# Kernel tuning notes

Measured on AMD Instinct MI355X. Metric: run time of the kernel, lower is better.

## Reference

```python
import jax, jax.numpy as jnp
import numpy as np

H = 8          # num_head
HD = 64        # head_dim = hidden_dim // num_head
WIN = 33       # atten_window_size (odd)
MIN_SCORE = -1e9


def setup_inputs() -> dict:
    key = jax.random.key(0)
    ks = jax.random.split(key, 12)
    B, S, D = 8, 4096, 512
    scale = 1.0 / np.sqrt(D).astype(np.float32)

    def lin_w(k):
        return jax.random.normal(k, (D, D), jnp.float32) * scale

    return {
        "query": jax.random.normal(ks[0], (B, S, D), jnp.float32),
        "key": jax.random.normal(ks[1], (B, S, D), jnp.float32),
        "value": jax.random.normal(ks[2], (B, S, D), jnp.float32),
        "mask": jax.random.randint(ks[3], (B, S), 0, 2).astype(bool),
        "Wq": lin_w(ks[4]), "bq": jax.random.normal(ks[5], (D,), jnp.float32) * 0.02,
        "Wk": lin_w(ks[6]), "bk": jax.random.normal(ks[7], (D,), jnp.float32) * 0.02,
        "Wv": lin_w(ks[8]), "bv": jax.random.normal(ks[9], (D,), jnp.float32) * 0.02,
        "Wo": lin_w(ks[10]), "bo": jax.random.normal(ks[11], (D,), jnp.float32) * 0.02,
    }


def reference(query, key, value, mask, Wq, bq, Wk, bk, Wv, bv, Wo, bo):
    B, S, D = query.shape
    half = min(WIN // 2, S // 2)

    def proj_split(x, W, b):
        # nn.Linear: x @ W.T + b; then split heads and flatten (B,H) -> B*H
        y = x @ W.T + b
        return y.reshape(B, S, H, HD).transpose(0, 2, 1, 3).reshape(B * H, S, HD)

    q = proj_split(query, Wq, bq)   # [BH, S, HD]
    k = proj_split(key, Wk, bk)
    v = proj_split(value, Wv, bv)
    # mask expanded over heads; True = masked (LocalAttention semantics)
    m = jnp.broadcast_to(mask[:, None, :], (B, H, S)).reshape(B * H, S)

    # banded scores: one [BH, S] vector per window offset (no sqrt(head_dim) scaling,
    # faithful to LocalAttention)
    scores = []
    for off in range(-half, half + 1):
        if off < 0:
            w = jnp.sum(q[:, -off:] * k[:, :off], axis=-1)
            w = jnp.where(m[:, :off], MIN_SCORE, w)
            w = jnp.pad(w, ((0, 0), (-off, 0)), constant_values=MIN_SCORE)
        elif off == 0:
            w = jnp.where(m, MIN_SCORE, jnp.sum(q * k, axis=-1))
        else:
            w = jnp.sum(q[:, :-off] * k[:, off:], axis=-1)
            w = jnp.where(m[:, off:], MIN_SCORE, w)
            w = jnp.pad(w, ((0, 0), (0, off)), constant_values=MIN_SCORE)
        scores.append(w)
    probs = jax.nn.softmax(jnp.stack(scores, axis=-1), axis=-1)  # [BH, S, 2*half+1]

    # weighted gather of values along the band (dropout=0 -> identity)
    out = jnp.zeros_like(v)
    for i, off in enumerate(range(-half, half + 1)):
        p = probs[:, :, i:i + 1]
        if off < 0:
            out = out + jnp.pad(p[:, -off:] * v[:, :off], ((0, 0), (-off, 0), (0, 0)))
        elif off == 0:
            out = out + p * v
        else:
            out = out + jnp.pad(p[:, :-off] * v[:, off:], ((0, 0), (0, off), (0, 0)))

    out = out.reshape(B, H, S, HD).transpose(0, 2, 1, 3).reshape(B, S, D)
    return out @ Wo.T + bo
```

## Files before the change

### kernel.cpp

```cpp
#include <hip/hip_runtime.h>
#include <hip/hip_bf16.h>
#include <stdint.h>

#define BB 8
#define SS 4096
#define DD 512
#define HH 8
#define HDIM 64

typedef unsigned short u16;
typedef __attribute__((ext_vector_type(4))) float f32x4;
typedef __attribute__((ext_vector_type(4))) short s16x4;
typedef __attribute__((ext_vector_type(8))) short s16x8;
typedef __attribute__((ext_vector_type(4))) unsigned int u32x4;

__device__ __forceinline__ u16 f2bf(float f) {
  uint32_t x = __builtin_bit_cast(uint32_t, f);
  x += 0x7fffu + ((x >> 16) & 1u);
  return (u16)(x >> 16);
}
__device__ __forceinline__ float bf2f(u16 u) {
  uint32_t x = (uint32_t)u << 16;
  return __builtin_bit_cast(float, x);
}
__device__ __forceinline__ uint32_t cvtpk(float a, float b) {
  uint32_t d;
  asm("v_cvt_pk_bf16_f32 %0, %1, %2" : "=v"(d) : "v"(a), "v"(b));
  return d;
}

__device__ __forceinline__ void gld_lds16(const void* g, void* l) {
  __builtin_amdgcn_global_load_lds((const __attribute__((address_space(1))) void*)g,
                                   (__attribute__((address_space(3))) void*)l, 16, 0, 0);
}

__global__ void cvt_weights(const float* __restrict__ w0, const float* __restrict__ w1,
                            const float* __restrict__ w2, const float* __restrict__ w3,
                            u16* __restrict__ out) {
  int i = blockIdx.x * blockDim.x + threadIdx.x;
  const int n = DD * DD;
  if (i < n) {
    out[i]         = f2bf(w0[i]);
    out[n + i]     = f2bf(w1[i]);
    out[2 * n + i] = f2bf(w2[i]);
    out[3 * n + i] = f2bf(w3[i]);
  }
}

__global__ void mask_unpack(const void* __restrict__ mraw, uint8_t* __restrict__ mk, int n) {
  __shared__ int bad[3];
  __shared__ int mode;
  const int t = threadIdx.x;
  if (t < 3) bad[t] = 0;
  __syncthreads();
  const uint32_t* w = (const uint32_t*)mraw;
  const uint32_t x = w[t];
  const bool w01 = (x == 0u) || (x == 1u);
  const uint32_t ob = x | (x >> 8) | (x >> 16) | (x >> 24);
  const bool u01 = ((ob & 0xFEu) == 0u);
  if (!w01) atomicAdd(&bad[0], 1);
  if (!u01) atomicAdd(&bad[1], 1);
  __syncthreads();
  if (t == 0) mode = (bad[0] == 0) ? 0 : (bad[1] == 0 ? 1 : 2);
  __syncthreads();
  const int md = mode;
  for (int i = blockIdx.x * 256 + t; i < n; i += gridDim.x * 256) {
    uint8_t v;
    if (md == 0)      v = (uint8_t)(w[i] & 1u);
    else if (md == 1) v = ((const uint8_t*)mraw)[i] ? 1 : 0;
    else              v = (w[i] != 0u) ? 1 : 0;
    mk[i] = v;
  }
}

template <typename TA, typename TC>
__global__ __launch_bounds__(256, 2)
void gemm97(const TA* __restrict__ A, const u16* __restrict__ Bw,
            const float* __restrict__ bias, TC* __restrict__ C,
            int M, int N, int K) {
  constexpr bool AF32 = (sizeof(TA) == 4);
  constexpr int ABYTES = AF32 ? 128 * 64 * 4 : 128 * 64 * 2;
  __shared__ __align__(16) char sA[ABYTES];
  __shared__ __align__(16) u16 sB[128 * 64];

  const int tid = threadIdx.x;
  const int lane = tid & 63, wv = tid >> 6;
  const int wr = (wv >> 1) * 64, wc = (wv & 1) * 64;
  const int c = lane & 15, g = lane >> 4;
  const int lid = blockIdx.x;
  const int rb = (lid >> 5) * 8 + (lid & 7);
  const int cb = (lid >> 3) & 3;
  const int col0 = cb * 128, row0 = rb * 128;

  const int srB = tid >> 3, cBc = (tid & 7) ^ ((tid >> 3) & 7);
  const u16* b_src = Bw + (size_t)(col0 + srB) * K + cBc * 8;
  const int srA = tid >> 4, cAc = (tid & 15) ^ (tid >> 4);
  const TA* a_srcF = A + (size_t)(row0 + srA) * K + cAc * 4;
  const TA* a_srcH = A + (size_t)(row0 + srB) * K + cBc * 8;

  f32x4 acc[4][4];
#pragma unroll
  for (int a = 0; a < 4; ++a)
#pragma unroll
    for (int b = 0; b < 4; ++b) acc[a][b] = (f32x4){0.f, 0.f, 0.f, 0.f};

  const int nkt = K / 64;
  for (int kt = 0; kt < nkt; ++kt) {
    __syncthreads();
    const int ko = kt * 64;
    if constexpr (AF32) {
#pragma unroll
      for (int i = 0; i < 8; ++i)
        gld_lds16(a_srcF + (size_t)i * 16 * K + ko, sA + i * 4096 + wv * 1024);
    } else {
#pragma unroll
      for (int i = 0; i < 4; ++i)
        gld_lds16(a_srcH + (size_t)i * 32 * K + ko, sA + i * 4096 + wv * 1024);
    }
#pragma unroll
    for (int i = 0; i < 4; ++i)
      gld_lds16(b_src + (size_t)i * 32 * K + ko, (char*)sB + i * 4096 + wv * 1024);
    __syncthreads();

#pragma unroll
    for (int ks = 0; ks < 2; ++ks) {
      s16x8 af[4], bq[4];
#pragma unroll
      for (int mf = 0; mf < 4; ++mf) {
        const int row = wr + mf * 16 + c;
        if constexpr (AF32) {
          const int bc = ks * 128 + g * 32;
          const f32x4 lo4 = *(const f32x4*)(sA + row * 256 + ((bc) ^ (c << 4)));
          const f32x4 hi4 = *(const f32x4*)(sA + row * 256 + ((bc + 16) ^ (c << 4)));
          const u32x4 dd = (u32x4){cvtpk(lo4[0], lo4[1]), cvtpk(lo4[2], lo4[3]),
                                   cvtpk(hi4[0], hi4[1]), cvtpk(hi4[2], hi4[3])};
          af[mf] = __builtin_bit_cast(s16x8, dd);
        } else {
          const int bc = ks * 64 + g * 16;
          af[mf] = *(const s16x8*)(sA + row * 128 + (bc ^ ((c & 7) << 4)));
        }
      }
#pragma unroll
      for (int nf = 0; nf < 4; ++nf) {
        const int row = wc + nf * 16 + c;
        const int bc = ks * 64 + g * 16;
        bq[nf] = *(const s16x8*)((char*)sB + row * 128 + (bc ^ ((c & 7) << 4)));
      }
#pragma unroll
      for (int mf = 0; mf < 4; ++mf)
#pragma unroll
        for (int nf = 0; nf < 4; ++nf)
          acc[mf][nf] = __builtin_amdgcn_mfma_f32_16x16x32_bf16(af[mf], bq[nf], acc[mf][nf], 0, 0, 0);
    }
  }

#pragma unroll
  for (int nf = 0; nf < 4; ++nf) {
    const int col = col0 + wc + nf * 16 + c;
    const float bv = bias[col];
#pragma unroll
    for (int mf = 0; mf < 4; ++mf) {
#pragma unroll
      for (int i = 0; i < 4; ++i) {
        const int row = row0 + wr + mf * 16 + g * 4 + i;
        const float v = acc[mf][nf][i] + bv;
        if constexpr (sizeof(TC) == 4) C[(size_t)row * N + col] = v;
        else                           C[(size_t)row * N + col] = (TC)f2bf(v);
      }
    }
  }
}

__device__ __forceinline__ void hilo8(const f32x4& a0, const f32x4& a1, s16x8& h, s16x8& l) {
#pragma unroll
  for (int j = 0; j < 4; ++j) {
    const float f = a0[j];
    const u16 hb = f2bf(f);
    h[j] = (short)hb;
    l[j] = (short)f2bf(f - bf2f(hb));
  }
#pragma unroll
  for (int j = 0; j < 4; ++j) {
    const float f = a1[j];
    const u16 hb = f2bf(f);
    h[4 + j] = (short)hb;
    l[4 + j] = (short)f2bf(f - bf2f(hb));
  }
}

#define ACH 4

__global__ __launch_bounds__(256, 4)
void attn_mfma(const float* __restrict__ Qp, const float* __restrict__ Kp,
               const u16* __restrict__ Vp, const uint8_t* __restrict__ mk,
               u16* __restrict__ O) {
  __shared__ u16 sKh[96 * 72];
  __shared__ u16 sKl[96 * 68];
  __shared__ u16 sVT[64 * 104];
  __shared__ u16 sM[96];

  const int bh = blockIdx.x;
  const int b = bh >> 3, h = bh & 7;
  const int base0 = blockIdx.y * (64 * ACH);
  const int tid = threadIdx.x;

  const int wv = tid >> 6, lane = tid & 63;
  const int c = lane & 15, g = lane >> 4;
  const int qloc = wv * 16 + c;

  const int krow0 = tid >> 3, kj = tid & 7;
  const int kks = kj >> 2, kg2 = kj & 3;
  const int vk0 = tid >> 3, vdg8 = tid & 7;

  f32x4 kA0[3], kA1[3];
  s16x8 vR[3];
  u16 mR = 1;
  f32x4 qn0[2], qn1[2];

  auto issue_loads = [&](int cs) {
#pragma unroll
    for (int it = 0; it < 3; ++it) {
      const int row = krow0 + it * 32;
      const int gr = cs - 16 + row;
      if (gr >= 0 && gr < SS) {
        const float* kp = Kp + ((size_t)(b * SS + gr)) * DD + h * HDIM + kks * 32 + kg2 * 4;
        kA0[it] = *(const f32x4*)kp;
        kA1[it] = *(const f32x4*)(kp + 16);
      } else {
        kA0[it] = (f32x4){0.f, 0.f, 0.f, 0.f};
        kA1[it] = (f32x4){0.f, 0.f, 0.f, 0.f};
      }
    }
#pragma unroll
    for (int it = 0; it < 3; ++it) {
      const int k = vk0 + it * 32;
      const int gr = cs - 16 + k;
      if (gr >= 0 && gr < SS)
        vR[it] = *(const s16x8*)(Vp + ((size_t)(b * SS + gr)) * DD + h * HDIM + vdg8 * 8);
      else
        vR[it] = (s16x8){0, 0, 0, 0, 0, 0, 0, 0};
    }
    if (tid < 96) {
      const int gr = cs - 16 + tid;
      mR = (gr < 0 || gr >= SS || mk[b * SS + gr]) ? 1 : 0;
    }
    const float* qp = Qp + ((size_t)(b * SS + cs + qloc)) * DD + h * HDIM;
#pragma unroll
    for (int ks = 0; ks < 2; ++ks) {
      qn0[ks] = *(const f32x4*)(qp + 32 * ks + 4 * g);
      qn1[ks] = *(const f32x4*)(qp + 32 * ks + 16 + 4 * g);
    }
  };

  auto write_stage = [&]() {
#pragma unroll
    for (int it = 0; it < 3; ++it) {
      const int row = krow0 + it * 32;
      s16x8 hh, ll;
      hilo8(kA0[it], kA1[it], hh, ll);
      *(s16x8*)&sKh[row * 72 + kj * 8] = hh;
      *(s16x4*)&sKl[row * 68 + kj * 8]     = (s16x4){ll[0], ll[1], ll[2], ll[3]};
      *(s16x4*)&sKl[row * 68 + kj * 8 + 4] = (s16x4){ll[4], ll[5], ll[6], ll[7]};
    }
#pragma unroll
    for (int it = 0; it < 3; ++it) {
      const int k = vk0 + it * 32;
      const int ks = k >> 5, rem = k & 31, hf = rem >> 4, q = rem & 15;
      const int g2 = q >> 2, i2 = q & 3;
      const int pos = (ks * 4 + g2) * 8 + hf * 4 + i2;
#pragma unroll
      for (int i = 0; i < 8; ++i) sVT[(vdg8 * 8 + i) * 104 + pos] = (u16)vR[it][i];
    }
    if (tid < 96) sM[tid] = mR;
  };

  issue_loads(base0);
  write_stage();
  __syncthreads();

  for (int t = 0; t < ACH; ++t) {
    const int s0 = base0 + t * 64;
    const int qrow = s0 + qloc;

    s16x8 qh[2], qlo[2];
#pragma unroll
    for (int ks = 0; ks < 2; ++ks) hilo8(qn0[ks], qn1[ks], qh[ks], qlo[ks]);

    if (t + 1 < ACH) issue_loads(base0 + (t + 1) * 64);

    f32x4 st[6];
#pragma unroll
    for (int kt = 0; kt < 6; ++kt) st[kt] = (f32x4){0.f, 0.f, 0.f, 0.f};
#pragma unroll
    for (int kt = 0; kt < 6; ++kt) {
      const int rb72 = (kt * 16 + c) * 72;
      const int rb68 = (kt * 16 + c) * 68;
#pragma unroll
      for (int ks = 0; ks < 2; ++ks) {
        const s16x8 kh = *(const s16x8*)&sKh[rb72 + ks * 32 + g * 8];
        const s16x4 l0 = *(const s16x4*)&sKl[rb68 + ks * 32 + g * 8];
        const s16x4 l1 = *(const s16x4*)&sKl[rb68 + ks * 32 + g * 8 + 4];
        const s16x8 kl = (s16x8){l0[0], l0[1], l0[2], l0[3], l1[0], l1[1], l1[2], l1[3]};
        st[kt] = __builtin_amdgcn_mfma_f32_16x16x32_bf16(kh, qh[ks], st[kt], 0, 0, 0);
        st[kt] = __builtin_amdgcn_mfma_f32_16x16x32_bf16(kh, qlo[ks], st[kt], 0, 0, 0);
        st[kt] = __builtin_amdgcn_mfma_f32_16x16x32_bf16(kl, qh[ks], st[kt], 0, 0, 0);
      }
    }

    float mx = -3.0e9f;
#pragma unroll
    for (int kt = 0; kt < 6; ++kt) {
#pragma unroll
      for (int i = 0; i < 4; ++i) {
        const int kl_ = kt * 16 + 4 * g + i;
        const int delta = kl_ - 16 - qloc;
        float v;
        if (delta < -16 || delta > 16) v = -2.0e9f;
        else if (sM[kl_])              v = -1.0e9f;
        else                           v = st[kt][i];
        st[kt][i] = v;
        mx = fmaxf(mx, v);
      }
    }
    mx = fmaxf(mx, __shfl_xor(mx, 16));
    mx = fmaxf(mx, __shfl_xor(mx, 32));
    float sum = 0.f;
#pragma unroll
    for (int kt = 0; kt < 6; ++kt) {
#pragma unroll
      for (int i = 0; i < 4; ++i) {
        const float e = __expf(st[kt][i] - mx);
        st[kt][i] = e;
        sum += e;
      }
    }
    sum += __shfl_xor(sum, 16);
    sum += __shfl_xor(sum, 32);
    const float inv = 1.f / sum;

    s16x8 ph[3];
#pragma unroll
    for (int ks = 0; ks < 3; ++ks) {
#pragma unroll
      for (int i = 0; i < 4; ++i) {
        ph[ks][i]     = (short)f2bf(st[2 * ks][i]);
        ph[ks][4 + i] = (short)f2bf(st[2 * ks + 1][i]);
      }
    }

    f32x4 ot[4];
#pragma unroll
    for (int dt = 0; dt < 4; ++dt) ot[dt] = (f32x4){0.f, 0.f, 0.f, 0.f};
#pragma unroll
    for (int dt = 0; dt < 4; ++dt) {
      const int rbv = (dt * 16 + c) * 104;
#pragma unroll
      for (int ks = 0; ks < 3; ++ks) {
        const s16x8 vh = *(const s16x8*)&sVT[rbv + ks * 32 + g * 8];
        ot[dt] = __builtin_amdgcn_mfma_f32_16x16x32_bf16(vh, ph[ks], ot[dt], 0, 0, 0);
      }
    }

    u16* op = O + ((size_t)(b * SS + qrow)) * DD + h * HDIM;
#pragma unroll
    for (int dt = 0; dt < 4; ++dt) {
      s16x4 pk;
#pragma unroll
      for (int i = 0; i < 4; ++i) pk[i] = (short)f2bf(ot[dt][i] * inv);
      *(s16x4*)&op[dt * 16 + 4 * g] = pk;
    }

    __syncthreads();
    if (t + 1 < ACH) {
      write_stage();
      __syncthreads();
    }
  }
}

__global__ __launch_bounds__(256)
void attn_win(const u16* __restrict__ Qp, const u16* __restrict__ Kp,
              const u16* __restrict__ Vp, const uint8_t* __restrict__ mk,
              u16* __restrict__ O) {
  constexpr int KR = 96;
  __shared__ float sK[KR][HDIM];
  __shared__ float sV[KR][HDIM];
  __shared__ float sMf[KR];

  const int bh = blockIdx.x;
  const int b = bh >> 3, h = bh & 7;
  const int s0 = blockIdx.y * 64;
  const int tid = threadIdx.x;

  for (int c = tid; c < KR * 16; c += 256) {
    const int row = c >> 4, c4 = c & 15;
    const int gr = s0 - 16 + row;
    float kv[4], vv[4];
    if (gr >= 0 && gr < SS) {
      const size_t base = ((size_t)(b * SS + gr)) * DD + h * HDIM + c4 * 4;
      const s16x4 kk = *(const s16x4*)(Kp + base);
      const s16x4 vx = *(const s16x4*)(Vp + base);
#pragma unroll
      for (int i = 0; i < 4; ++i) { kv[i] = bf2f((u16)kk[i]); vv[i] = bf2f((u16)vx[i]); }
    } else {
#pragma unroll
      for (int i = 0; i < 4; ++i) { kv[i] = 0.f; vv[i] = 0.f; }
    }
#pragma unroll
    for (int i = 0; i < 4; ++i) {
      const int d = c4 * 4 + i;
      const int pd = (d & 15) * 4 + (d >> 4);
      sK[row][pd] = kv[i];
      sV[row][pd] = vv[i];
    }
  }
  for (int r = tid; r < KR; r += 256) {
    const int gr = s0 - 16 + r;
    sMf[r] = (gr < 0 || gr >= SS || mk[b * SS + gr]) ? 1.f : 0.f;
  }
  __syncthreads();

  const int wv = tid >> 6, lane = tid & 63;
  const int g = lane >> 4, d16 = lane & 15;

  for (int rr = 0; rr < 16; rr += 4) {
    const int lr = wv * 16 + rr + g;
    const int srow = s0 + lr;
    const u16* qp = Qp + ((size_t)(b * SS + srow)) * DD + h * HDIM;
    float q0 = bf2f(qp[d16]), q1 = bf2f(qp[d16 + 16]), q2 = bf2f(qp[d16 + 32]), q3 = bf2f(qp[d16 + 48]);
    float sc[33];
#pragma unroll
    for (int o = 0; o < 33; ++o) {
      const f32x4 kk = *(const f32x4*)&sK[lr + o][d16 * 4];
      float p = q0 * kk[0] + q1 * kk[1] + q2 * kk[2] + q3 * kk[3];
      p += __shfl_xor(p, 1);
      p += __shfl_xor(p, 2);
      p += __shfl_xor(p, 4);
      p += __shfl_xor(p, 8);
      sc[o] = (sMf[lr + o] != 0.f) ? -1.0e9f : p;
    }
    float mx = sc[0];
#pragma unroll
    for (int o = 1; o < 33; ++o) mx = fmaxf(mx, sc[o]);
    float sum = 0.f;
#pragma unroll
    for (int o = 0; o < 33; ++o) { const float e = __expf(sc[o] - mx); sc[o] = e; sum += e; }
    const float inv = 1.f / sum;
    f32x4 acc = (f32x4){0.f, 0.f, 0.f, 0.f};
#pragma unroll
    for (int o = 0; o < 33; ++o) {
      const f32x4 vx = *(const f32x4*)&sV[lr + o][d16 * 4];
      acc += (sc[o] * inv) * vx;
    }
    u16* op = O + ((size_t)(b * SS + srow)) * DD + h * HDIM;
    op[d16]      = f2bf(acc[0]);
    op[d16 + 16] = f2bf(acc[1]);
    op[d16 + 32] = f2bf(acc[2]);
    op[d16 + 48] = f2bf(acc[3]);
  }
}

extern "C" void kernel_launch(void* const* d_in, const int* in_sizes, int n_in,
                              void* d_out, int out_size, void* d_ws, size_t ws_size,
                              hipStream_t stream) {
  const float* query = (const float*)d_in[0];
  const float* key   = (const float*)d_in[1];
  const float* value = (const float*)d_in[2];
  const void*  mraw  = d_in[3];
  const float* Wq = (const float*)d_in[4];
  const float* bq = (const float*)d_in[5];
  const float* Wk = (const float*)d_in[6];
  const float* bk = (const float*)d_in[7];
  const float* Wv = (const float*)d_in[8];
  const float* bv = (const float*)d_in[9];
  const float* Wo = (const float*)d_in[10];
  const float* bo = (const float*)d_in[11];

  const int M = BB * SS, N = DD, K = DD;

  char* ws = (char*)d_ws;
  size_t off = 0;
  auto carve = [&](size_t bytes) -> char* {
    char* p = ws + off;
    off = (off + bytes + 255) & ~(size_t)255;
    return p;
  };
  u16* wAll   = (u16*)carve((size_t)4 * DD * DD * sizeof(u16));
  uint8_t* mk = (uint8_t*)carve((size_t)BB * SS);

  const size_t qk_f32 = (size_t)M * DD * 4;
  const size_t v_b16  = (size_t)M * DD * 2;
  const bool f32p = (off + 2 * qk_f32 + 2 * v_b16 + 1024) <= ws_size;

  cvt_weights<<<(DD * DD + 255) / 256, 256, 0, stream>>>(Wq, Wk, Wv, Wo, wAll);
  mask_unpack<<<16, 256, 0, stream>>>(mraw, mk, BB * SS);

  const dim3 gg((M / 128) * (N / 128));
  const dim3 ga(BB * HH, SS / (64 * ACH));

  if (f32p) {
    float* Qf = (float*)carve(qk_f32);
    float* Kf = (float*)carve(qk_f32);
    u16*   Vb = (u16*)carve(v_b16);
    u16*   AO = (u16*)carve(v_b16);
    gemm97<float, float><<<gg, 256, 0, stream>>>(query, wAll,               bq, Qf, M, N, K);
    gemm97<float, float><<<gg, 256, 0, stream>>>(key,   wAll + DD * DD,     bk, Kf, M, N, K);
    gemm97<float, u16><<<gg, 256, 0, stream>>>(value, wAll + 2 * DD * DD, bv, Vb, M, N, K);
    attn_mfma<<<ga, 256, 0, stream>>>(Qf, Kf, Vb, mk, AO);
    gemm97<u16, float><<<gg, 256, 0, stream>>>(AO, wAll + 3 * DD * DD, bo, (float*)d_out, M, N, K);
  } else {
    const dim3 ga1(BB * HH, SS / 64);
    u16* Qb = (u16*)carve(v_b16);
    u16* Kb = (u16*)carve(v_b16);
    u16* Vb = (u16*)carve(v_b16);
    u16* AO = (u16*)carve(v_b16);
    gemm97<float, u16><<<gg, 256, 0, stream>>>(query, wAll,               bq, Qb, M, N, K);
    gemm97<float, u16><<<gg, 256, 0, stream>>>(key,   wAll + DD * DD,     bk, Kb, M, N, K);
    gemm97<float, u16><<<gg, 256, 0, stream>>>(value, wAll + 2 * DD * DD, bv, Vb, M, N, K);
    attn_win<<<ga1, 256, 0, stream>>>(Qb, Kb, Vb, mk, AO);
    gemm97<u16, float><<<gg, 256, 0, stream>>>(AO, wAll + 3 * DD * DD, bo, (float*)d_out, M, N, K);
  }
}
```

Baseline: 228.5 us.

## Register-stage fp32 A tiles as bf16 in GEMM and XOR-swizzle attention LDS

The GEMM's fp32 A-operand path now loads the next tile into registers while the current tile is computed, converts it to bf16 once, and stores it to a swizzled bf16 LDS buffer. This halves A's LDS footprint and lets launch bounds rise to three blocks per CU. The attention kernel replaces padded LDS rows for K-hi, K-lo and transposed V with XOR-swizzled unpadded rows, so the K-lo operand comes from a single 16-byte read. It also raises wave priority around the MFMA sections. The risks are more register pressure from prefetching in the GEMM and a V-transpose scatter that may still hit bank conflicts.

```diff
diff --git a/kernel.cpp b/kernel.cpp
--- a/kernel.cpp
+++ b/kernel.cpp
@@ -74,13 +74,12 @@
 }
 
 template <typename TA, typename TC>
-__global__ __launch_bounds__(256, 2)
+__global__ __launch_bounds__(256, 3)
 void gemm97(const TA* __restrict__ A, const u16* __restrict__ Bw,
             const float* __restrict__ bias, TC* __restrict__ C,
             int M, int N, int K) {
   constexpr bool AF32 = (sizeof(TA) == 4);
-  constexpr int ABYTES = AF32 ? 128 * 64 * 4 : 128 * 64 * 2;
-  __shared__ __align__(16) char sA[ABYTES];
+  __shared__ __align__(16) u16 sA2[128 * 64];
   __shared__ __align__(16) u16 sB[128 * 64];
 
   const int tid = threadIdx.x;
@@ -94,57 +93,63 @@
 
   const int srB = tid >> 3, cBc = (tid & 7) ^ ((tid >> 3) & 7);
   const u16* b_src = Bw + (size_t)(col0 + srB) * K + cBc * 8;
-  const int srA = tid >> 4, cAc = (tid & 15) ^ (tid >> 4);
-  const TA* a_srcF = A + (size_t)(row0 + srA) * K + cAc * 4;
   const TA* a_srcH = A + (size_t)(row0 + srB) * K + cBc * 8;
 
+  const int ar = tid >> 1, ah = tid & 1;
+  const TA* a_srcF = A + (size_t)(row0 + ar) * K + ah * 32;
+
+  f32x4 aR[8];
+  auto loadA = [&](int ko) {
+    if constexpr (AF32) {
+#pragma unroll
+      for (int q = 0; q < 8; ++q) aR[q] = *(const f32x4*)(a_srcF + ko + q * 4);
+    }
+  };
+
   f32x4 acc[4][4];
 #pragma unroll
   for (int a = 0; a < 4; ++a)
 #pragma unroll
     for (int b = 0; b < 4; ++b) acc[a][b] = (f32x4){0.f, 0.f, 0.f, 0.f};
 
+  loadA(0);
   const int nkt = K / 64;
   for (int kt = 0; kt < nkt; ++kt) {
+    const int ko = kt * 64;
     __syncthreads();
-    const int ko = kt * 64;
     if constexpr (AF32) {
 #pragma unroll
-      for (int i = 0; i < 8; ++i)
-        gld_lds16(a_srcF + (size_t)i * 16 * K + ko, sA + i * 4096 + wv * 1024);
+      for (int j2 = 0; j2 < 4; ++j2) {
+        const int j = ah * 4 + j2;
+        const f32x4 v0 = aR[2 * j2], v1 = aR[2 * j2 + 1];
+        const u32x4 dd = (u32x4){cvtpk(v0[0], v0[1]), cvtpk(v0[2], v0[3]),
+                                 cvtpk(v1[0], v1[1]), cvtpk(v1[2], v1[3])};
+        *(s16x8*)&sA2[ar * 64 + (j ^ (ar & 7)) * 8] = __builtin_bit_cast(s16x8, dd);
+      }
     } else {
 #pragma unroll
       for (int i = 0; i < 4; ++i)
-        gld_lds16(a_srcH + (size_t)i * 32 * K + ko, sA + i * 4096 + wv * 1024);
+        gld_lds16(a_srcH + (size_t)i * 32 * K + ko, (char*)sA2 + i * 4096 + wv * 1024);
     }
 #pragma unroll
     for (int i = 0; i < 4; ++i)
       gld_lds16(b_src + (size_t)i * 32 * K + ko, (char*)sB + i * 4096 + wv * 1024);
     __syncthreads();
 
+    if (kt + 1 < nkt) loadA(ko + 64);
+
 #pragma unroll
     for (int ks = 0; ks < 2; ++ks) {
       s16x8 af[4], bq[4];
 #pragma unroll
       for (int mf = 0; mf < 4; ++mf) {
         const int row = wr + mf * 16 + c;
-        if constexpr (AF32) {
-          const int bc = ks * 128 + g * 32;
-          const f32x4 lo4 = *(const f32x4*)(sA + row * 256 + ((bc) ^ (c << 4)));
-          const f32x4 hi4 = *(const f32x4*)(sA + row * 256 + ((bc + 16) ^ (c << 4)));
-          const u32x4 dd = (u32x4){cvtpk(lo4[0], lo4[1]), cvtpk(lo4[2], lo4[3]),
-                                   cvtpk(hi4[0], hi4[1]), cvtpk(hi4[2], hi4[3])};
-          af[mf] = __builtin_bit_cast(s16x8, dd);
-        } else {
-          const int bc = ks * 64 + g * 16;
-          af[mf] = *(const s16x8*)(sA + row * 128 + (bc ^ ((c & 7) << 4)));
-        }
+        af[mf] = *(const s16x8*)&sA2[row * 64 + ((ks * 4 + g) ^ (c & 7)) * 8];
       }
 #pragma unroll
       for (int nf = 0; nf < 4; ++nf) {
         const int row = wc + nf * 16 + c;
-        const int bc = ks * 64 + g * 16;
-        bq[nf] = *(const s16x8*)((char*)sB + row * 128 + (bc ^ ((c & 7) << 4)));
+        bq[nf] = *(const s16x8*)&sB[row * 64 + ((ks * 4 + g) ^ (c & 7)) * 8];
       }
 #pragma unroll
       for (int mf = 0; mf < 4; ++mf)
@@ -194,9 +199,9 @@
 void attn_mfma(const float* __restrict__ Qp, const float* __restrict__ Kp,
                const u16* __restrict__ Vp, const uint8_t* __restrict__ mk,
                u16* __restrict__ O) {
-  __shared__ u16 sKh[96 * 72];
-  __shared__ u16 sKl[96 * 68];
-  __shared__ u16 sVT[64 * 104];
+  __shared__ u16 sKh[96 * 64];
+  __shared__ u16 sKl[96 * 64];
+  __shared__ u16 sVT[64 * 128];
   __shared__ u16 sM[96];
 
   const int bh = blockIdx.x;
@@ -258,18 +263,21 @@
       const int row = krow0 + it * 32;
       s16x8 hh, ll;
       hilo8(kA0[it], kA1[it], hh, ll);
-      *(s16x8*)&sKh[row * 72 + kj * 8] = hh;
-      *(s16x4*)&sKl[row * 68 + kj * 8]     = (s16x4){ll[0], ll[1], ll[2], ll[3]};
-      *(s16x4*)&sKl[row * 68 + kj * 8 + 4] = (s16x4){ll[4], ll[5], ll[6], ll[7]};
+      const int slot = kj ^ (row & 7);
+      *(s16x8*)&sKh[row * 64 + slot * 8] = hh;
+      *(s16x8*)&sKl[row * 64 + slot * 8] = ll;
     }
 #pragma unroll
     for (int it = 0; it < 3; ++it) {
       const int k = vk0 + it * 32;
       const int ks = k >> 5, rem = k & 31, hf = rem >> 4, q = rem & 15;
       const int g2 = q >> 2, i2 = q & 3;
-      const int pos = (ks * 4 + g2) * 8 + hf * 4 + i2;
-#pragma unroll
-      for (int i = 0; i < 8; ++i) sVT[(vdg8 * 8 + i) * 104 + pos] = (u16)vR[it][i];
+      const int j = ks * 4 + g2, off = hf * 4 + i2;
+#pragma unroll
+      for (int i = 0; i < 8; ++i) {
+        const int d = vdg8 * 8 + i;
+        sVT[d * 128 + ((j ^ (d & 7)) * 8) + off] = (u16)vR[it][i];
+      }
     }
     if (tid < 96) sM[tid] = mR;
   };
@@ -291,21 +299,21 @@
     f32x4 st[6];
 #pragma unroll
     for (int kt = 0; kt < 6; ++kt) st[kt] = (f32x4){0.f, 0.f, 0.f, 0.f};
+    __builtin_amdgcn_s_setprio(1);
 #pragma unroll
     for (int kt = 0; kt < 6; ++kt) {
-      const int rb72 = (kt * 16 + c) * 72;
-      const int rb68 = (kt * 16 + c) * 68;
+      const int base = (kt * 16 + c) * 64;
 #pragma unroll
       for (int ks = 0; ks < 2; ++ks) {
-        const s16x8 kh = *(const s16x8*)&sKh[rb72 + ks * 32 + g * 8];
-        const s16x4 l0 = *(const s16x4*)&sKl[rb68 + ks * 32 + g * 8];
-        const s16x4 l1 = *(const s16x4*)&sKl[rb68 + ks * 32 + g * 8 + 4];
-        const s16x8 kl = (s16x8){l0[0], l0[1], l0[2], l0[3], l1[0], l1[1], l1[2], l1[3]};
+        const int slot = (ks * 4 + g) ^ (c & 7);
+        const s16x8 kh = *(const s16x8*)&sKh[base + slot * 8];
+        const s16x8 kl = *(const s16x8*)&sKl[base + slot * 8];
         st[kt] = __builtin_amdgcn_mfma_f32_16x16x32_bf16(kh, qh[ks], st[kt], 0, 0, 0);
         st[kt] = __builtin_amdgcn_mfma_f32_16x16x32_bf16(kh, qlo[ks], st[kt], 0, 0, 0);
         st[kt] = __builtin_amdgcn_mfma_f32_16x16x32_bf16(kl, qh[ks], st[kt], 0, 0, 0);
       }
     }
+    __builtin_amdgcn_s_setprio(0);
 
     float mx = -3.0e9f;
 #pragma unroll
@@ -351,15 +359,17 @@
     f32x4 ot[4];
 #pragma unroll
     for (int dt = 0; dt < 4; ++dt) ot[dt] = (f32x4){0.f, 0.f, 0.f, 0.f};
+    __builtin_amdgcn_s_setprio(1);
 #pragma unroll
     for (int dt = 0; dt < 4; ++dt) {
-      const int rbv = (dt * 16 + c) * 104;
+      const int rbv = (dt * 16 + c) * 128;
 #pragma unroll
       for (int ks = 0; ks < 3; ++ks) {
-        const s16x8 vh = *(const s16x8*)&sVT[rbv + ks * 32 + g * 8];
+        const s16x8 vh = *(const s16x8*)&sVT[rbv + (((ks * 4 + g) ^ (c & 7)) * 8)];
         ot[dt] = __builtin_amdgcn_mfma_f32_16x16x32_bf16(vh, ph[ks], ot[dt], 0, 0, 0);
       }
     }
+    __builtin_amdgcn_s_setprio(0);
 
     u16* op = O + ((size_t)(b * SS + qrow)) * DD + h * HDIM;
 #pragma unroll
```

Result: slower. 270.6 us (+18.4%).

## Restrict each wave's QK and PV MFMAs to its 48-key band window

Applied to the files above, without the earlier changes.

Each wave now computes scores only against the 48 keys around its 16 queries (rows kb..kb+47), not all 96 staged keys. This halves the QK MFMAs and cuts the PV MFMAs from 12 to 8, with the last half-tile zero-padded. The V-transpose layout becomes plain key-major with stride 100 so waves can read an offset window, and s_setprio is raised around the MFMA blocks. The risk is LDS bank conflicts from the new stride and unaligned 4-element reads.

```diff
diff --git a/kernel.cpp b/kernel.cpp
--- a/kernel.cpp
+++ b/kernel.cpp
@@ -189,6 +189,7 @@
 }
 
 #define ACH 4
+#define VSTR 100
 
 __global__ __launch_bounds__(256, 4)
 void attn_mfma(const float* __restrict__ Qp, const float* __restrict__ Kp,
@@ -196,7 +197,7 @@
                u16* __restrict__ O) {
   __shared__ u16 sKh[96 * 72];
   __shared__ u16 sKl[96 * 68];
-  __shared__ u16 sVT[64 * 104];
+  __shared__ u16 sVT[64 * VSTR];
   __shared__ u16 sM[96];
 
   const int bh = blockIdx.x;
@@ -207,6 +208,7 @@
   const int wv = tid >> 6, lane = tid & 63;
   const int c = lane & 15, g = lane >> 4;
   const int qloc = wv * 16 + c;
+  const int kb = wv * 16;
 
   const int krow0 = tid >> 3, kj = tid & 7;
   const int kks = kj >> 2, kg2 = kj & 3;
@@ -265,11 +267,9 @@
 #pragma unroll
     for (int it = 0; it < 3; ++it) {
       const int k = vk0 + it * 32;
-      const int ks = k >> 5, rem = k & 31, hf = rem >> 4, q = rem & 15;
-      const int g2 = q >> 2, i2 = q & 3;
-      const int pos = (ks * 4 + g2) * 8 + hf * 4 + i2;
-#pragma unroll
-      for (int i = 0; i < 8; ++i) sVT[(vdg8 * 8 + i) * 104 + pos] = (u16)vR[it][i];
+#pragma unroll
+      for (int i = 0; i < 8; ++i)
+        sVT[(vdg8 * 8 + i) * VSTR + k] = (u16)vR[it][i];
     }
     if (tid < 96) sM[tid] = mR;
   };
@@ -288,13 +288,15 @@
 
     if (t + 1 < ACH) issue_loads(base0 + (t + 1) * 64);
 
-    f32x4 st[6];
-#pragma unroll
-    for (int kt = 0; kt < 6; ++kt) st[kt] = (f32x4){0.f, 0.f, 0.f, 0.f};
-#pragma unroll
-    for (int kt = 0; kt < 6; ++kt) {
-      const int rb72 = (kt * 16 + c) * 72;
-      const int rb68 = (kt * 16 + c) * 68;
+    f32x4 st[3];
+#pragma unroll
+    for (int kt = 0; kt < 3; ++kt) st[kt] = (f32x4){0.f, 0.f, 0.f, 0.f};
+    __builtin_amdgcn_s_setprio(1);
+#pragma unroll
+    for (int kt = 0; kt < 3; ++kt) {
+      const int krow = kb + kt * 16 + c;
+      const int rb72 = krow * 72;
+      const int rb68 = krow * 68;
 #pragma unroll
       for (int ks = 0; ks < 2; ++ks) {
         const s16x8 kh = *(const s16x8*)&sKh[rb72 + ks * 32 + g * 8];
@@ -306,17 +308,18 @@
         st[kt] = __builtin_amdgcn_mfma_f32_16x16x32_bf16(kl, qh[ks], st[kt], 0, 0, 0);
       }
     }
+    __builtin_amdgcn_s_setprio(0);
 
     float mx = -3.0e9f;
 #pragma unroll
-    for (int kt = 0; kt < 6; ++kt) {
+    for (int kt = 0; kt < 3; ++kt) {
 #pragma unroll
       for (int i = 0; i < 4; ++i) {
-        const int kl_ = kt * 16 + 4 * g + i;
-        const int delta = kl_ - 16 - qloc;
+        const int delta = kt * 16 + 4 * g + i - 16 - c;
+        const int key = kb + kt * 16 + 4 * g + i;
         float v;
         if (delta < -16 || delta > 16) v = -2.0e9f;
-        else if (sM[kl_])              v = -1.0e9f;
+        else if (sM[key])              v = -1.0e9f;
         else                           v = st[kt][i];
         st[kt][i] = v;
         mx = fmaxf(mx, v);
@@ -326,7 +329,7 @@
     mx = fmaxf(mx, __shfl_xor(mx, 32));
     float sum = 0.f;
 #pragma unroll
-    for (int kt = 0; kt < 6; ++kt) {
+    for (int kt = 0; kt < 3; ++kt) {
 #pragma unroll
       for (int i = 0; i < 4; ++i) {
         const float e = __expf(st[kt][i] - mx);
@@ -338,28 +341,31 @@
     sum += __shfl_xor(sum, 32);
     const float inv = 1.f / sum;
 
-    s16x8 ph[3];
-#pragma unroll
-    for (int ks = 0; ks < 3; ++ks) {
-#pragma unroll
-      for (int i = 0; i < 4; ++i) {
-        ph[ks][i]     = (short)f2bf(st[2 * ks][i]);
-        ph[ks][4 + i] = (short)f2bf(st[2 * ks + 1][i]);
-      }
+    s16x8 ph[2];
+#pragma unroll
+    for (int i = 0; i < 4; ++i) {
+      ph[0][i]     = (short)f2bf(st[0][i]);
+      ph[0][4 + i] = (short)f2bf(st[1][i]);
+      ph[1][i]     = (short)f2bf(st[2][i]);
+      ph[1][4 + i] = 0;
     }
 
     f32x4 ot[4];
 #pragma unroll
     for (int dt = 0; dt < 4; ++dt) ot[dt] = (f32x4){0.f, 0.f, 0.f, 0.f};
+    __builtin_amdgcn_s_setprio(1);
 #pragma unroll
     for (int dt = 0; dt < 4; ++dt) {
-      const int rbv = (dt * 16 + c) * 104;
-#pragma unroll
-      for (int ks = 0; ks < 3; ++ks) {
-        const s16x8 vh = *(const s16x8*)&sVT[rbv + ks * 32 + g * 8];
-        ot[dt] = __builtin_amdgcn_mfma_f32_16x16x32_bf16(vh, ph[ks], ot[dt], 0, 0, 0);
-      }
-    }
+      const int rowb = (dt * 16 + c) * VSTR;
+      const s16x4 v0 = *(const s16x4*)&sVT[rowb + kb + 4 * g];
+      const s16x4 v1 = *(const s16x4*)&sVT[rowb + kb + 16 + 4 * g];
+      const s16x8 vh0 = (s16x8){v0[0], v0[1], v0[2], v0[3], v1[0], v1[1], v1[2], v1[3]};
+      ot[dt] = __builtin_amdgcn_mfma_f32_16x16x32_bf16(vh0, ph[0], ot[dt], 0, 0, 0);
+      const s16x4 v2 = *(const s16x4*)&sVT[rowb + kb + 32 + 4 * g];
+      const s16x8 vh1 = (s16x8){v2[0], v2[1], v2[2], v2[3], 0, 0, 0, 0};
+      ot[dt] = __builtin_amdgcn_mfma_f32_16x16x32_bf16(vh1, ph[1], ot[dt], 0, 0, 0);
+    }
+    __builtin_amdgcn_s_setprio(0);
 
     u16* op = O + ((size_t)(b * SS + qrow)) * DD + h * HDIM;
 #pragma unroll
```

Measured after the change: 224.4 us. No clear change (-1.8%).
